# Kernel tuning notes

Measured on AMD Instinct MI355X. Metric: run time of the kernel, lower is better.

The kernel has to match this reference:

```python
import jax, jax.numpy as jnp
import numpy as np
from jax.ops import segment_sum

N = 102400          # num nodes
E = 1638400         # num edges (avg degree 16)
F_IN = 128          # node_feature_dim
H = 128             # hidden_dim
L = 2               # num_layers
B = 64              # num graphs
NPG = N // B        # nodes per graph (equal-size graphs -> static dense shape)


def setup_inputs() -> dict:
    key = jax.random.key(0)
    ks = jax.random.split(key, 8)
    x = jax.random.normal(ks[0], (N, F_IN), dtype=jnp.float32)
    edge_index = jax.random.randint(ks[1], (2, E), 0, N, dtype=jnp.int64)
    batch = (jnp.arange(N, dtype=jnp.int64) // NPG)  # sorted, equal-size graphs
    s_in = 1.0 / np.sqrt(F_IN)
    s_h = 1.0 / np.sqrt(H)
    W_in = jax.random.uniform(ks[2], (F_IN, H), jnp.float32, -s_in, s_in)
    b_in = jax.random.uniform(ks[3], (H,), jnp.float32, -s_in, s_in)
    Ws = jax.random.uniform(ks[4], (L, H, H), jnp.float32, -s_h, s_h)
    bs = jax.random.uniform(ks[5], (L, H), jnp.float32, -s_h, s_h)
    return {"x": x, "edge_index": edge_index, "batch": batch,
            "W_in": W_in, "b_in": b_in, "Ws": Ws, "bs": bs}


def _gcn_conv(x, W, b, src, dst):
    # PyG GCNConv: self-loops + symmetric deg^-1/2 normalization + scatter-add
    h = x @ W                                            # [N, H]
    loops = jnp.arange(N, dtype=src.dtype)
    s = jnp.concatenate([src, loops])                    # [E+N]
    d = jnp.concatenate([dst, loops])
    deg = segment_sum(jnp.ones_like(d, dtype=h.dtype), d, num_segments=N)
    dinv = jnp.where(deg > 0, jax.lax.rsqrt(deg), 0.0)   # deg^-0.5, inf->0
    norm = dinv[s] * dinv[d]                             # [E+N]
    msg = h[s] * norm[:, None]                           # gather + scale
    out = segment_sum(msg, d, num_segments=N)            # scatter-add at target
    return out + b


def reference(x, edge_index, batch, W_in, b_in, Ws, bs):
    src, dst = edge_index[0], edge_index[1]
    h = x @ W_in + b_in                                  # node_feature_transform
    for l in range(L):
        h = jax.nn.relu(_gcn_conv(h, Ws[l], bs[l], src, dst))
        # dropout(0.1) is identity in eval mode
    # to_dense_batch: batch is sorted with exactly NPG nodes per graph
    dense = h.reshape(B, NPG, H)                          # [B, max_nodes, H]
    return dense
```

## Files before the change

kernel.cpp:

```cpp
#include <hip/hip_runtime.h>
#include <hip/hip_bf16.h>

#define NNODES 102400
#define NEDGES 1638400
#define HD 128
#define ZROW_OFF (NNODES * 256)

#define NB 128
#define NT 512
#define EPB (NEDGES / NB)
#define EIT (EPB / NT)
#define NSLICE 8
#define SLICE (NNODES / NSLICE)

typedef float f32x4 __attribute__((ext_vector_type(4)));
typedef short short8 __attribute__((ext_vector_type(8)));
typedef unsigned short ushort8 __attribute__((ext_vector_type(8)));
typedef unsigned int uint32;

static __device__ __forceinline__ unsigned short f2bf(float v) {
  union { float f; unsigned u; } x; x.f = v;
  unsigned r = x.u + 0x7fffu + ((x.u >> 16) & 1u);
  return (unsigned short)(r >> 16);
}
static __device__ __forceinline__ float bflo(uint32 u) { return __uint_as_float(u << 16); }
static __device__ __forceinline__ float bfhi(uint32 u) { return __uint_as_float(u & 0xffff0000u); }

__global__ __launch_bounds__(NT) void k_hist(const int* __restrict__ dst,
                                             unsigned short* __restrict__ blkcnt,
                                             unsigned short* __restrict__ lrank16) {
  __shared__ int hist[SLICE];
  const int blk = blockIdx.x, tid = threadIdx.x;
  const int e0 = blk * EPB;
  int dreg[EIT];
  #pragma unroll
  for (int i = 0; i < EIT; ++i) dreg[i] = dst[e0 + i * NT + tid];

  for (int p = 0; p < NSLICE; ++p) {
    const int lo = p * SLICE;
    for (int i = tid; i < SLICE; i += NT) hist[i] = 0;
    __syncthreads();
    #pragma unroll
    for (int i = 0; i < EIT; ++i) {
      int r = dreg[i] - lo;
      if ((unsigned)r < (unsigned)SLICE) {
        int lr = atomicAdd(&hist[r], 1);
        lrank16[e0 + i * NT + tid] = (unsigned short)lr;
      }
    }
    __syncthreads();
    for (int i = tid; i < SLICE; i += NT)
      blkcnt[(size_t)blk * NNODES + lo + i] = (unsigned short)hist[i];
    __syncthreads();
  }
}

__global__ __launch_bounds__(256) void k_scan1(unsigned short* __restrict__ blkcnt,
                                               int* __restrict__ rowptr, int* __restrict__ partials,
                                               float* __restrict__ dinv, int* __restrict__ degs) {
  __shared__ int s[256];
  int t = threadIdx.x;
  int i = blockIdx.x * 256 + t;
  int run = 0;
  #pragma unroll 8
  for (int b = 0; b < NB; ++b) {
    size_t idx = (size_t)b * NNODES + i;
    int c = blkcnt[idx];
    blkcnt[idx] = (unsigned short)run;
    run += c;
  }
  degs[i] = run;
  dinv[i] = rsqrtf((float)run + 1.0f);
  int vp = (run + 3) & ~3;
  s[t] = vp; __syncthreads();
  for (int off = 1; off < 256; off <<= 1) {
    int x = (t >= off) ? s[t - off] : 0;
    __syncthreads();
    s[t] += x; __syncthreads();
  }
  rowptr[i] = s[t] - vp;
  if (t == 255) partials[blockIdx.x] = s[t];
}

__global__ __launch_bounds__(512) void k_scan2(int* __restrict__ partials) {
  __shared__ int s[512];
  int t = threadIdx.x;
  int v = (t < 400) ? partials[t] : 0;
  s[t] = v; __syncthreads();
  for (int off = 1; off < 512; off <<= 1) {
    int x = (t >= off) ? s[t - off] : 0;
    __syncthreads();
    s[t] += x; __syncthreads();
  }
  if (t < 400) partials[t] = s[t] - v;
}

__global__ __launch_bounds__(256) void k_scan3(int* __restrict__ rowptr, const int* __restrict__ partials,
                                               const int* __restrict__ degs, int* __restrict__ csr) {
  int i = blockIdx.x * 256 + threadIdx.x;
  int base = rowptr[i] + partials[blockIdx.x];
  rowptr[i] = base;
  int v = degs[i];
  int vp = (v + 3) & ~3;
  for (int t = v; t < vp; ++t) csr[base + t] = ZROW_OFF;
  if (i == NNODES - 1) rowptr[NNODES] = base + vp;
}

__global__ __launch_bounds__(256) void k_fill(const int* __restrict__ src, const int* __restrict__ dst,
                                              const unsigned short* __restrict__ lrank16,
                                              const int* __restrict__ rowptr,
                                              const unsigned short* __restrict__ blkcnt,
                                              int* __restrict__ csr) {
  int e = blockIdx.x * 256 + threadIdx.x;
  int s = src[e], d = dst[e];
  int b = e / EPB;
  int slot = rowptr[d] + (int)blkcnt[(size_t)b * NNODES + d] + (int)lrank16[e];
  csr[slot] = s * 256;
}

__global__ __launch_bounds__(256) void k_prep(const float* __restrict__ W_in, const float* __restrict__ Ws,
                                              const float* __restrict__ b_in,
                                              unsigned short* __restrict__ WT0, unsigned short* __restrict__ WT1,
                                              float* __restrict__ bc) {
  int blk = blockIdx.x, tid = threadIdx.x;
  if (blk < 64) {
    int t = blk * 256 + tid;
    int c = t >> 7, k = t & 127;
    float acc = 0.f;
    #pragma unroll 4
    for (int j = 0; j < 128; ++j) acc += W_in[k * 128 + j] * Ws[j * 128 + c];
    WT0[c * 128 + k] = f2bf(acc);
  } else if (blk == 64) {
    if (tid < 128) {
      float acc = 0.f;
      #pragma unroll 4
      for (int j = 0; j < 128; ++j) acc += b_in[j] * Ws[j * 128 + tid];
      bc[tid] = acc;
    }
  } else {
    int t = (blk - 65) * 256 + tid;
    int c = t >> 7, k = t & 127;
    WT1[c * 128 + k] = f2bf(Ws[128 * 128 + k * 128 + c]);
  }
}

template<bool IN_F32, bool ADD_BIAS, bool SCALE>
__global__ __launch_bounds__(256) void k_gemm(const void* __restrict__ inp, const unsigned short* __restrict__ WT,
                                              const float* __restrict__ bias, const float* __restrict__ dinv,
                                              unsigned short* __restrict__ outp) {
  __shared__ unsigned short sA[128][136];
  __shared__ unsigned short sB[128][136];
  const int tid = threadIdx.x;
  const size_t r0 = (size_t)blockIdx.x * 128;

  #pragma unroll
  for (int i = 0; i < 8; ++i) {
    int f = tid + i * 256;
    int c = f >> 4, u = f & 15;
    *(ushort8*)&sB[c][u * 8] = *(const ushort8*)&WT[(size_t)c * 128 + u * 8];
  }
  if constexpr (IN_F32) {
    const float* in = (const float*)inp;
    #pragma unroll
    for (int i = 0; i < 8; ++i) {
      int f = tid + i * 256;
      int row = f >> 4, u = f & 15;
      const float4 v0 = *(const float4*)&in[(r0 + row) * 128 + u * 8];
      const float4 v1 = *(const float4*)&in[(r0 + row) * 128 + u * 8 + 4];
      ushort8 pk;
      pk[0] = f2bf(v0.x); pk[1] = f2bf(v0.y); pk[2] = f2bf(v0.z); pk[3] = f2bf(v0.w);
      pk[4] = f2bf(v1.x); pk[5] = f2bf(v1.y); pk[6] = f2bf(v1.z); pk[7] = f2bf(v1.w);
      *(ushort8*)&sA[row][u * 8] = pk;
    }
  } else {
    const unsigned short* in = (const unsigned short*)inp;
    #pragma unroll
    for (int i = 0; i < 8; ++i) {
      int f = tid + i * 256;
      int row = f >> 4, u = f & 15;
      *(ushort8*)&sA[row][u * 8] = *(const ushort8*)&in[(r0 + row) * 128 + u * 8];
    }
  }
  __syncthreads();

  const int lane = tid & 63;
  const int wv = tid >> 6;
  const int wr = wv >> 1, wc = wv & 1;
  const int lrow = lane & 15, lg = lane >> 4;

  f32x4 acc[4][4];
  #pragma unroll
  for (int m = 0; m < 4; ++m)
    #pragma unroll
    for (int n = 0; n < 4; ++n)
      acc[m][n] = (f32x4){0.f, 0.f, 0.f, 0.f};

  #pragma unroll
  for (int kt = 0; kt < 4; ++kt) {
    short8 a[4], b[4];
    #pragma unroll
    for (int m = 0; m < 4; ++m)
      a[m] = *(const short8*)&sA[wr * 64 + m * 16 + lrow][kt * 32 + lg * 8];
    #pragma unroll
    for (int n = 0; n < 4; ++n)
      b[n] = *(const short8*)&sB[wc * 64 + n * 16 + lrow][kt * 32 + lg * 8];
    #pragma unroll
    for (int m = 0; m < 4; ++m)
      #pragma unroll
      for (int n = 0; n < 4; ++n)
        acc[m][n] = __builtin_amdgcn_mfma_f32_16x16x32_bf16(a[m], b[n], acc[m][n], 0, 0, 0);
  }

  #pragma unroll
  for (int m = 0; m < 4; ++m) {
    size_t row0 = r0 + wr * 64 + m * 16 + lg * 4;
    float4 dv = {1.f, 1.f, 1.f, 1.f};
    if constexpr (SCALE) dv = *(const float4*)&dinv[row0];
    #pragma unroll
    for (int n = 0; n < 4; ++n) {
      int col = wc * 64 + n * 16 + lrow;
      float bv = ADD_BIAS ? bias[col] : 0.0f;
      f32x4 v = acc[m][n];
      #pragma unroll
      for (int r = 0; r < 4; ++r) {
        float o = v[r] + bv;
        if constexpr (SCALE) o *= ((const float*)&dv)[r];
        outp[(row0 + r) * 128 + col] = f2bf(o);
      }
    }
  }
}

template<bool OUT_F32>
__global__ __launch_bounds__(256) void k_agg(const unsigned short* __restrict__ g, const int* __restrict__ csr,
                                             const int* __restrict__ rowptr, const float* __restrict__ dinv,
                                             const float* __restrict__ bias, void* __restrict__ outp) {
  int n = blockIdx.x * 4 + (threadIdx.x >> 6);
  int lane = threadIdx.x & 63;
  const char* gb = (const char*)g;
  const int lo4 = lane * 4;

  uint32 sv = *(const uint32*)(gb + (size_t)(n * 256 + lo4));
  float accx = bflo(sv), accy = bfhi(sv);
  int j = rowptr[n], je = rowptr[n + 1];

#define LD(off) (*(const uint32*)(gb + (size_t)(unsigned)((off) + lo4)))
  for (; j + 16 <= je; j += 16) {
    int4 c0 = *(const int4*)&csr[j];
    int4 c1 = *(const int4*)&csr[j + 4];
    int4 c2 = *(const int4*)&csr[j + 8];
    int4 c3 = *(const int4*)&csr[j + 12];
    uint32 q0 = LD(c0.x), q1 = LD(c0.y), q2 = LD(c0.z), q3 = LD(c0.w);
    uint32 q4 = LD(c1.x), q5 = LD(c1.y), q6 = LD(c1.z), q7 = LD(c1.w);
    uint32 q8 = LD(c2.x), q9 = LD(c2.y), qa = LD(c2.z), qb = LD(c2.w);
    uint32 qc = LD(c3.x), qd = LD(c3.y), qe = LD(c3.z), qf = LD(c3.w);
    accx += bflo(q0) + bflo(q1) + bflo(q2) + bflo(q3)
          + bflo(q4) + bflo(q5) + bflo(q6) + bflo(q7)
          + bflo(q8) + bflo(q9) + bflo(qa) + bflo(qb)
          + bflo(qc) + bflo(qd) + bflo(qe) + bflo(qf);
    accy += bfhi(q0) + bfhi(q1) + bfhi(q2) + bfhi(q3)
          + bfhi(q4) + bfhi(q5) + bfhi(q6) + bfhi(q7)
          + bfhi(q8) + bfhi(q9) + bfhi(qa) + bfhi(qb)
          + bfhi(qc) + bfhi(qd) + bfhi(qe) + bfhi(qf);
  }
  if (j + 8 <= je) {
    int4 c0 = *(const int4*)&csr[j];
    int4 c1 = *(const int4*)&csr[j + 4];
    uint32 q0 = LD(c0.x), q1 = LD(c0.y), q2 = LD(c0.z), q3 = LD(c0.w);
    uint32 q4 = LD(c1.x), q5 = LD(c1.y), q6 = LD(c1.z), q7 = LD(c1.w);
    accx += bflo(q0) + bflo(q1) + bflo(q2) + bflo(q3)
          + bflo(q4) + bflo(q5) + bflo(q6) + bflo(q7);
    accy += bfhi(q0) + bfhi(q1) + bfhi(q2) + bfhi(q3)
          + bfhi(q4) + bfhi(q5) + bfhi(q6) + bfhi(q7);
    j += 8;
  }
  if (j + 4 <= je) {
    int4 c0 = *(const int4*)&csr[j];
    uint32 q0 = LD(c0.x), q1 = LD(c0.y), q2 = LD(c0.z), q3 = LD(c0.w);
    accx += bflo(q0) + bflo(q1) + bflo(q2) + bflo(q3);
    accy += bfhi(q0) + bfhi(q1) + bfhi(q2) + bfhi(q3);
  }
#undef LD

  float dn = dinv[n];
  float2 b2 = ((const float2*)bias)[lane];
  accx = fmaxf(fmaf(accx, dn, b2.x), 0.0f);
  accy = fmaxf(fmaf(accy, dn, b2.y), 0.0f);
  if constexpr (OUT_F32) {
    ((float2*)outp)[(size_t)n * 64 + lane] = make_float2(accx, accy);
  } else {
    uint32 pk = ((uint32)f2bf(accy) << 16) | (uint32)f2bf(accx);
    ((uint32*)outp)[(size_t)n * 64 + lane] = pk;
  }
}

extern "C" void kernel_launch(void* const* d_in, const int* in_sizes, int n_in,
                              void* d_out, int out_size, void* d_ws, size_t ws_size,
                              hipStream_t stream) {
  const float* x    = (const float*)d_in[0];
  const int*   ei   = (const int*)d_in[1];
  const float* W_in = (const float*)d_in[3];
  const float* b_in = (const float*)d_in[4];
  const float* Ws   = (const float*)d_in[5];
  const float* bs   = (const float*)d_in[6];
  float* out = (float*)d_out;
  const int* src = ei;
  const int* dst = ei + NEDGES;

  char* ws = (char*)d_ws;
  size_t off = 0;
  auto alloc = [&](size_t bytes) { void* p = ws + off; off = (off + bytes + 255) & ~(size_t)255; return p; };
  unsigned short* Bb  = (unsigned short*)alloc((size_t)NNODES * 128 * 2 + 512);
  unsigned short* A   = (unsigned short*)alloc((size_t)NNODES * 128 * 2);
  unsigned short* WT0 = (unsigned short*)alloc((size_t)128 * 128 * 2);
  unsigned short* WT1 = (unsigned short*)alloc((size_t)128 * 128 * 2);
  float* bc      = (float*)alloc(128 * 4);
  int*   rowptr  = (int*)alloc((size_t)(NNODES + 1) * 4);
  int*   partials= (int*)alloc(512 * 4);
  float* dinv    = (float*)alloc((size_t)NNODES * 4);
  int*   degs    = (int*)alloc((size_t)NNODES * 4);
  int*   csr     = (int*)alloc((size_t)(NEDGES + 3 * NNODES) * 4);
  unsigned short* blkcnt  = (unsigned short*)Bb;
  unsigned short* lrank16 = (unsigned short*)A;

  hipMemsetAsync(Bb + (size_t)NNODES * 128, 0, 512, stream);
  k_hist <<<NB, NT, 0, stream>>>(dst, blkcnt, lrank16);
  k_scan1<<<NNODES / 256, 256, 0, stream>>>(blkcnt, rowptr, partials, dinv, degs);
  k_scan2<<<1, 512, 0, stream>>>(partials);
  k_scan3<<<NNODES / 256, 256, 0, stream>>>(rowptr, partials, degs, csr);
  k_fill <<<NEDGES / 256, 256, 0, stream>>>(src, dst, lrank16, rowptr, blkcnt, csr);
  k_prep <<<129, 256, 0, stream>>>(W_in, Ws, b_in, WT0, WT1, bc);

  k_gemm<true, true, true><<<NNODES / 128, 256, 0, stream>>>(x, WT0, bc, dinv, Bb);
  k_agg<false><<<NNODES / 4, 256, 0, stream>>>(Bb, csr, rowptr, dinv, bs, A);
  k_gemm<false, false, true><<<NNODES / 128, 256, 0, stream>>>(A, WT1, nullptr, dinv, Bb);
  k_agg<true><<<NNODES / 4, 256, 0, stream>>>(Bb, csr, rowptr, dinv, bs + 128, out);
}
```

Measured before the change: 347.3 us.

## Collapse CSR build into fewer kernels with atomic block offsets and start/end rows

Replaces the three-kernel prefix scan with a single scan that reserves each block's base offset through a global atomic counter. Rows are stored as (start,end) pairs, so the scan no longer has to be globally ordered. The weight-prep work is folded into extra blocks of the same launch, and the memset moves into k_hist. k_fill is remapped so each block works within one histogram block, and NSLICE drops from 8 to 5, giving fewer histogram passes but a larger shared-memory histogram. The aim is to cut launch count and serialization in preprocessing, at the cost of a nondeterministic CSR row order and lower occupancy in k_hist.

```diff
diff --git a/kernel.cpp b/kernel.cpp
--- a/kernel.cpp
+++ b/kernel.cpp
@@ -10,8 +10,10 @@
 #define NT 512
 #define EPB (NEDGES / NB)
 #define EIT (EPB / NT)
-#define NSLICE 8
+#define NSLICE 5
 #define SLICE (NNODES / NSLICE)
+
+#define SCAN_BLOCKS 400
 
 typedef float f32x4 __attribute__((ext_vector_type(4)));
 typedef short short8 __attribute__((ext_vector_type(8)));
@@ -28,9 +30,14 @@
 
 __global__ __launch_bounds__(NT) void k_hist(const int* __restrict__ dst,
                                              unsigned short* __restrict__ blkcnt,
-                                             unsigned short* __restrict__ lrank16) {
+                                             unsigned short* __restrict__ lrank16,
+                                             int* __restrict__ gctr) {
   __shared__ int hist[SLICE];
   const int blk = blockIdx.x, tid = threadIdx.x;
+  if (blk == 0) {
+    if (tid == 0) *gctr = 0;
+    if (tid < 128) ((uint32*)((char*)blkcnt + ZROW_OFF))[tid] = 0;
+  }
   const int e0 = blk * EPB;
   int dreg[EIT];
   #pragma unroll
@@ -55,12 +62,40 @@
   }
 }
 
-__global__ __launch_bounds__(256) void k_scan1(unsigned short* __restrict__ blkcnt,
-                                               int* __restrict__ rowptr, int* __restrict__ partials,
-                                               float* __restrict__ dinv, int* __restrict__ degs) {
+__global__ __launch_bounds__(256) void k_scanA(unsigned short* __restrict__ blkcnt,
+                                               int2* __restrict__ rowse, float* __restrict__ dinv,
+                                               int* __restrict__ csr, int* __restrict__ gctr,
+                                               const float* __restrict__ W_in, const float* __restrict__ Ws,
+                                               const float* __restrict__ b_in,
+                                               unsigned short* __restrict__ WT0,
+                                               unsigned short* __restrict__ WT1, float* __restrict__ bc) {
   __shared__ int s[256];
-  int t = threadIdx.x;
-  int i = blockIdx.x * 256 + t;
+  __shared__ int sbase;
+  const int bid = blockIdx.x, t = threadIdx.x;
+  if (bid >= SCAN_BLOCKS) {
+    int blk = bid - SCAN_BLOCKS;
+    if (blk < 64) {
+      int tt = blk * 256 + t;
+      int c = tt >> 7, k = tt & 127;
+      float acc = 0.f;
+      #pragma unroll 4
+      for (int j = 0; j < 128; ++j) acc += W_in[k * 128 + j] * Ws[j * 128 + c];
+      WT0[c * 128 + k] = f2bf(acc);
+    } else if (blk == 64) {
+      if (t < 128) {
+        float acc = 0.f;
+        #pragma unroll 4
+        for (int j = 0; j < 128; ++j) acc += b_in[j] * Ws[j * 128 + t];
+        bc[t] = acc;
+      }
+    } else {
+      int tt = (blk - 65) * 256 + t;
+      int c = tt >> 7, k = tt & 127;
+      WT1[c * 128 + k] = f2bf(Ws[128 * 128 + k * 128 + c]);
+    }
+    return;
+  }
+  int i = bid * 256 + t;
   int run = 0;
   #pragma unroll 8
   for (int b = 0; b < NB; ++b) {
@@ -69,7 +104,6 @@
     blkcnt[idx] = (unsigned short)run;
     run += c;
   }
-  degs[i] = run;
   dinv[i] = rsqrtf((float)run + 1.0f);
   int vp = (run + 3) & ~3;
   s[t] = vp; __syncthreads();
@@ -78,69 +112,28 @@
     __syncthreads();
     s[t] += x; __syncthreads();
   }
-  rowptr[i] = s[t] - vp;
-  if (t == 255) partials[blockIdx.x] = s[t];
-}
-
-__global__ __launch_bounds__(512) void k_scan2(int* __restrict__ partials) {
-  __shared__ int s[512];
-  int t = threadIdx.x;
-  int v = (t < 400) ? partials[t] : 0;
-  s[t] = v; __syncthreads();
-  for (int off = 1; off < 512; off <<= 1) {
-    int x = (t >= off) ? s[t - off] : 0;
-    __syncthreads();
-    s[t] += x; __syncthreads();
-  }
-  if (t < 400) partials[t] = s[t] - v;
-}
-
-__global__ __launch_bounds__(256) void k_scan3(int* __restrict__ rowptr, const int* __restrict__ partials,
-                                               const int* __restrict__ degs, int* __restrict__ csr) {
-  int i = blockIdx.x * 256 + threadIdx.x;
-  int base = rowptr[i] + partials[blockIdx.x];
-  rowptr[i] = base;
-  int v = degs[i];
-  int vp = (v + 3) & ~3;
-  for (int t = v; t < vp; ++t) csr[base + t] = ZROW_OFF;
-  if (i == NNODES - 1) rowptr[NNODES] = base + vp;
+  if (t == 255) sbase = atomicAdd(gctr, s[255]);
+  __syncthreads();
+  int base = sbase + s[t] - vp;
+  rowse[i] = make_int2(base, base + vp);
+  for (int q = run; q < vp; ++q) csr[base + q] = ZROW_OFF;
 }
 
 __global__ __launch_bounds__(256) void k_fill(const int* __restrict__ src, const int* __restrict__ dst,
                                               const unsigned short* __restrict__ lrank16,
-                                              const int* __restrict__ rowptr,
+                                              const int2* __restrict__ rowse,
                                               const unsigned short* __restrict__ blkcnt,
                                               int* __restrict__ csr) {
-  int e = blockIdx.x * 256 + threadIdx.x;
-  int s = src[e], d = dst[e];
-  int b = e / EPB;
-  int slot = rowptr[d] + (int)blkcnt[(size_t)b * NNODES + d] + (int)lrank16[e];
-  csr[slot] = s * 256;
-}
-
-__global__ __launch_bounds__(256) void k_prep(const float* __restrict__ W_in, const float* __restrict__ Ws,
-                                              const float* __restrict__ b_in,
-                                              unsigned short* __restrict__ WT0, unsigned short* __restrict__ WT1,
-                                              float* __restrict__ bc) {
-  int blk = blockIdx.x, tid = threadIdx.x;
-  if (blk < 64) {
-    int t = blk * 256 + tid;
-    int c = t >> 7, k = t & 127;
-    float acc = 0.f;
-    #pragma unroll 4
-    for (int j = 0; j < 128; ++j) acc += W_in[k * 128 + j] * Ws[j * 128 + c];
-    WT0[c * 128 + k] = f2bf(acc);
-  } else if (blk == 64) {
-    if (tid < 128) {
-      float acc = 0.f;
-      #pragma unroll 4
-      for (int j = 0; j < 128; ++j) acc += b_in[j] * Ws[j * 128 + tid];
-      bc[tid] = acc;
-    }
-  } else {
-    int t = (blk - 65) * 256 + tid;
-    int c = t >> 7, k = t & 127;
-    WT1[c * 128 + k] = f2bf(Ws[128 * 128 + k * 128 + c]);
+  int bid = blockIdx.x;
+  int part = bid >> 7;
+  int blk  = bid & 127;
+  const unsigned short* bc = blkcnt + (size_t)blk * NNODES;
+  int e0 = blk * EPB + part * 1280;
+  #pragma unroll
+  for (int it = 0; it < 5; ++it) {
+    int e = e0 + it * 256 + threadIdx.x;
+    int s = src[e], d = dst[e];
+    csr[rowse[d].x + (int)bc[d] + (int)lrank16[e]] = s * 256;
   }
 }
 
@@ -233,7 +226,7 @@
 
 template<bool OUT_F32>
 __global__ __launch_bounds__(256) void k_agg(const unsigned short* __restrict__ g, const int* __restrict__ csr,
-                                             const int* __restrict__ rowptr, const float* __restrict__ dinv,
+                                             const int2* __restrict__ rowse, const float* __restrict__ dinv,
                                              const float* __restrict__ bias, void* __restrict__ outp) {
   int n = blockIdx.x * 4 + (threadIdx.x >> 6);
   int lane = threadIdx.x & 63;
@@ -242,7 +235,8 @@
 
   uint32 sv = *(const uint32*)(gb + (size_t)(n * 256 + lo4));
   float accx = bflo(sv), accy = bfhi(sv);
-  int j = rowptr[n], je = rowptr[n + 1];
+  int2 se = rowse[n];
+  int j = se.x, je = se.y;
 
 #define LD(off) (*(const uint32*)(gb + (size_t)(unsigned)((off) + lo4)))
   for (; j + 16 <= je; j += 16) {
@@ -315,24 +309,20 @@
   unsigned short* WT0 = (unsigned short*)alloc((size_t)128 * 128 * 2);
   unsigned short* WT1 = (unsigned short*)alloc((size_t)128 * 128 * 2);
   float* bc      = (float*)alloc(128 * 4);
-  int*   rowptr  = (int*)alloc((size_t)(NNODES + 1) * 4);
-  int*   partials= (int*)alloc(512 * 4);
+  int2*  rowse   = (int2*)alloc((size_t)NNODES * 8);
+  int*   gctr    = (int*)alloc(256);
   float* dinv    = (float*)alloc((size_t)NNODES * 4);
-  int*   degs    = (int*)alloc((size_t)NNODES * 4);
   int*   csr     = (int*)alloc((size_t)(NEDGES + 3 * NNODES) * 4);
   unsigned short* blkcnt  = (unsigned short*)Bb;
   unsigned short* lrank16 = (unsigned short*)A;
 
-  hipMemsetAsync(Bb + (size_t)NNODES * 128, 0, 512, stream);
-  k_hist <<<NB, NT, 0, stream>>>(dst, blkcnt, lrank16);
-  k_scan1<<<NNODES / 256, 256, 0, stream>>>(blkcnt, rowptr, partials, dinv, degs);
-  k_scan2<<<1, 512, 0, stream>>>(partials);
-  k_scan3<<<NNODES / 256, 256, 0, stream>>>(rowptr, partials, degs, csr);
-  k_fill <<<NEDGES / 256, 256, 0, stream>>>(src, dst, lrank16, rowptr, blkcnt, csr);
-  k_prep <<<129, 256, 0, stream>>>(W_in, Ws, b_in, WT0, WT1, bc);
+  k_hist <<<NB, NT, 0, stream>>>(dst, blkcnt, lrank16, gctr);
+  k_scanA<<<SCAN_BLOCKS + 129, 256, 0, stream>>>(blkcnt, rowse, dinv, csr, gctr,
+                                                 W_in, Ws, b_in, WT0, WT1, bc);
+  k_fill <<<1280, 256, 0, stream>>>(src, dst, lrank16, rowse, blkcnt, csr);
 
   k_gemm<true, true, true><<<NNODES / 128, 256, 0, stream>>>(x, WT0, bc, dinv, Bb);
-  k_agg<false><<<NNODES / 4, 256, 0, stream>>>(Bb, csr, rowptr, dinv, bs, A);
+  k_agg<false><<<NNODES / 4, 256, 0, stream>>>(Bb, csr, rowse, dinv, bs, A);
   k_gemm<false, false, true><<<NNODES / 128, 256, 0, stream>>>(A, WT1, nullptr, dinv, Bb);
-  k_agg<true><<<NNODES / 4, 256, 0, stream>>>(Bb, csr, rowptr, dinv, bs + 128, out);
-}
+  k_agg<true><<<NNODES / 4, 256, 0, stream>>>(Bb, csr, rowse, dinv, bs + 128, out);
+}
```

Result: faster. 334.2 us (-3.8%).
